# Optimization experiments

Measured on AMD Instinct MI355X. Metric: run time of the kernel, lower is better.

Reference implementation:

```python
import jax, jax.numpy as jnp
import numpy as np

H = 128  # DECODER_LAYERS[0]
LN_EPS = 1e-3  # keras LayerNormalization default epsilon


def setup_inputs() -> dict:
    key = jax.random.key(0)
    ks = jax.random.split(key, 12)
    N_POS, N_COL, D = 1024, 512, 128
    n_seq = 8
    s = 1.0 / np.sqrt(D)
    h = 1.0 / np.sqrt(H)
    return {
        "seq_feat": jax.random.normal(ks[0], (N_POS, D), jnp.float32),
        "col_feat": jax.random.normal(ks[1], (N_COL, D), jnp.float32),
        "sequence_lengths": jnp.full((n_seq,), N_POS // n_seq, dtype=jnp.int32),
        "Ws": jax.random.normal(ks[2], (D, H), jnp.float32) * s,
        "bs": jnp.zeros((H,), jnp.float32),
        "Wc": jax.random.normal(ks[3], (D, H), jnp.float32) * s,
        "bc": jnp.zeros((H,), jnp.float32),
        "Wm": jax.random.normal(ks[4], (H, H), jnp.float32) * h,
        "bm": jnp.zeros((H,), jnp.float32),
        "gamma": jnp.ones((H,), jnp.float32),
        "beta": jnp.zeros((H,), jnp.float32),
        "Wo": jax.random.normal(ks[5], (H, 1), jnp.float32) * h,
        "bo": jnp.zeros((1,), jnp.float32),
    }


def reference(seq_feat, col_feat, sequence_lengths, Ws, bs, Wc, bc, Wm, bm, gamma, beta, Wo, bo):
    N_POS = seq_feat.shape[0]
    N_COL = col_feat.shape[0]
    n_seq = sequence_lengths.shape[0]

    seq_dec = jax.nn.relu(seq_feat @ Ws + bs)   # [N_pos, H]
    col_dec = jax.nn.relu(col_feat @ Wc + bc)   # [N_col, H]

    # broadcast outer-sum: [N_pos, N_col, H]
    logits = seq_dec[:, None, :] + col_dec[None, :, :]

    # MLP([128]): single Dense (no activation) + LayerNorm
    hmid = logits @ Wm + bm
    mu = jnp.mean(hmid, axis=-1, keepdims=True)
    var = jnp.mean(jnp.square(hmid - mu), axis=-1, keepdims=True)
    hln = (hmid - mu) / jnp.sqrt(var + LN_EPS) * gamma + beta

    raw = (hln @ Wo + bo)[..., 0]               # [N_pos, N_col]
    exp_logits = jnp.exp(raw)

    # column-axis normalization (softmax over last axis)
    M_c = exp_logits / jnp.sum(exp_logits, axis=-1, keepdims=True)

    # segment-ragged normalization over positions, per sequence
    segment_ids = jnp.repeat(jnp.arange(n_seq, dtype=jnp.int32), sequence_lengths,
                             total_repeat_length=N_POS)
    seg = jax.ops.segment_sum(exp_logits, segment_ids, num_segments=n_seq)  # [n_seq, N_col]
    M_s = exp_logits / seg[segment_ids]

    return M_c + M_s - M_c * M_s
```

## Files before the change

### kernel.cpp

```cpp
#include <hip/hip_runtime.h>

#define HDIM 128
#define NPOS 1024
#define NCOL 512
#define LN_EPS 1e-3f


__device__ __forceinline__ int seg_of(int i, const int* __restrict__ lens, int n_seq) {
    int cum = 0;
    for (int s = 0; s < n_seq; ++s) {
        cum += lens[s];
        if (i < cum) return s;
    }
    return n_seq - 1;
}

extern "C" __global__ void __launch_bounds__(512)
k1_precompute(const float* __restrict__ seq_feat, const float* __restrict__ col_feat,
              const float* __restrict__ Ws, const float* __restrict__ bsv,
              const float* __restrict__ Wc, const float* __restrict__ bcv,
              const float* __restrict__ Wm, const float* __restrict__ bmv,
              const float* __restrict__ gam, const float* __restrict__ Wo,
              const int* __restrict__ lens, int n_seq,
              float* __restrict__ AcT, float* __restrict__ BcT,
              float* __restrict__ p_arr, float* __restrict__ v_arr,
              float* __restrict__ q_arr, float* __restrict__ w_arr,
              float* __restrict__ sums, int* __restrict__ segid)
{
    __shared__ float xs[4][HDIM];
    __shared__ float ds_[4][HDIM];
    __shared__ float partm[8], partp[8], partv[8], mus[4];

    const int t    = threadIdx.x;
    const int b    = blockIdx.x;
    const int h    = t & 127;
    const int r    = t >> 7;
    const int wv   = t >> 6;
    const int lane = t & 63;

    {
        const int nsums = NPOS + n_seq * NCOL;
        int idx = b * 512 + t;
        if (idx < nsums) sums[idx] = 0.f;
        int idx2 = idx - nsums;
        if (idx2 >= 0 && idx2 < NPOS) segid[idx2] = seg_of(idx2, lens, n_seq);
    }

    const bool  is_seq = (b < NPOS / 4);
    const int   i0 = (is_seq ? b : (b - NPOS / 4)) * 4;
    const float* X  = is_seq ? seq_feat : col_feat;
    const float* W1 = is_seq ? Ws : Wc;
    const float* b1 = is_seq ? bsv : bcv;

    if (t < 128) {
        int rr = t >> 5, k4 = (t & 31) * 4;
        *(float4*)&xs[rr][k4] = *(const float4*)&X[(i0 + rr) * HDIM + k4];
    }
    __syncthreads();

    float d;
    {
        float a0 = 0.f, a1 = 0.f, a2 = 0.f, a3 = 0.f;
        #pragma unroll 8
        for (int k = 0; k < HDIM; k += 4) {
            float4 x = *(const float4*)&xs[r][k];
            float w0 = W1[(k + 0) * HDIM + h];
            float w1 = W1[(k + 1) * HDIM + h];
            float w2 = W1[(k + 2) * HDIM + h];
            float w3 = W1[(k + 3) * HDIM + h];
            a0 += x.x * w0; a1 += x.y * w1; a2 += x.z * w2; a3 += x.w * w3;
        }
        d = fmaxf(b1[h] + ((a0 + a1) + (a2 + a3)), 0.f);
    }
    ds_[r][h] = d;
    __syncthreads();

    float aa;
    {
        float a0 = 0.f, a1 = 0.f, a2 = 0.f, a3 = 0.f;
        #pragma unroll 8
        for (int k = 0; k < HDIM; k += 4) {
            float4 x = *(const float4*)&ds_[r][k];
            float w0 = Wm[(k + 0) * HDIM + h];
            float w1 = Wm[(k + 1) * HDIM + h];
            float w2 = Wm[(k + 2) * HDIM + h];
            float w3 = Wm[(k + 3) * HDIM + h];
            a0 += x.x * w0; a1 += x.y * w1; a2 += x.z * w2; a3 += x.w * w3;
        }
        aa = (is_seq ? 0.f : bmv[h]) + ((a0 + a1) + (a2 + a3));
    }

    {
        float s = aa;
        #pragma unroll
        for (int off = 32; off; off >>= 1) s += __shfl_xor(s, off, 64);
        if (lane == 0) partm[wv] = s;
    }
    __syncthreads();
    if (t < 4) mus[t] = (partm[2 * t] + partm[2 * t + 1]) * (1.f / HDIM);
    __syncthreads();

    const float a  = aa - mus[r];
    const float gw = gam[h] * Wo[h];

    {
        float sp = a * gw, sv = a * a;
        #pragma unroll
        for (int off = 32; off; off >>= 1) {
            sp += __shfl_xor(sp, off, 64);
            sv += __shfl_xor(sv, off, 64);
        }
        if (lane == 0) { partp[wv] = sp; partv[wv] = sv; }
    }
    xs[r][h] = a;
    __syncthreads();
    if (t < 4) {
        (is_seq ? p_arr : q_arr)[i0 + t] = partp[2 * t] + partp[2 * t + 1];
        (is_seq ? v_arr : w_arr)[i0 + t] = (partv[2 * t] + partv[2 * t + 1]) * (1.f / HDIM);
    }
    if (t < 128) {
        float4 st = make_float4(xs[0][t], xs[1][t], xs[2][t], xs[3][t]);
        if (is_seq) *(float4*)&AcT[t * NPOS + i0] = st;
        else        *(float4*)&BcT[t * NCOL + i0] = st;
    }
}

#define AS_STR 36
#define BS_STR 68

union K2Smem {
    struct { float As[128 * AS_STR]; float Bs[128 * BS_STR]; } s;
    struct { float comb[8 * 256]; float redr[512]; float redc[1024]; } r;
};

extern "C" __global__ void __launch_bounds__(512)
k2_gemm(const float* __restrict__ AcT, const float* __restrict__ BcT,
        const float* __restrict__ p_arr, const float* __restrict__ v_arr,
        const float* __restrict__ q_arr, const float* __restrict__ w_arr,
        const int* __restrict__ segid, int n_seq,
        float* __restrict__ E, float* __restrict__ rowsum, float* __restrict__ segsum)
{
    __shared__ K2Smem sm;

    const int t  = threadIdx.x;
    const int tt = t & 255;
    const int tc = tt & 15;
    const int tr = tt >> 4;
    const int kbase = (t >> 8) * 64;
    const int i0 = blockIdx.x * 32;
    const int j0 = blockIdx.y * 64;

    #pragma unroll
    for (int u = 0; u < 2; ++u) {
        int fid = t + 512 * u;
        int k = fid >> 3, m4 = fid & 7;
        *(float4*)&sm.s.As[k * AS_STR + 4 * m4] = *(const float4*)&AcT[k * NPOS + i0 + 4 * m4];
    }
    #pragma unroll
    for (int u = 0; u < 4; ++u) {
        int fid = t + 512 * u;
        int k = fid >> 4, n4 = fid & 15;
        *(float4*)&sm.s.Bs[k * BS_STR + 4 * n4] = *(const float4*)&BcT[k * NCOL + j0 + 4 * n4];
    }
    __syncthreads();

    float acc[8] = {0.f, 0.f, 0.f, 0.f, 0.f, 0.f, 0.f, 0.f};
    #pragma unroll 4
    for (int k = kbase; k < kbase + 64; ++k) {
        float2 a2 = *(const float2*)&sm.s.As[k * AS_STR + 2 * tr];
        float4 b4 = *(const float4*)&sm.s.Bs[k * BS_STR + 4 * tc];
        acc[0] += a2.x * b4.x; acc[1] += a2.x * b4.y; acc[2] += a2.x * b4.z; acc[3] += a2.x * b4.w;
        acc[4] += a2.y * b4.x; acc[5] += a2.y * b4.y; acc[6] += a2.y * b4.z; acc[7] += a2.y * b4.w;
    }

    const int seg_lo = segid[i0];
    const int seg_hi = segid[i0 + 31];
    __syncthreads();

    if (t >= 256) {
        #pragma unroll
        for (int j = 0; j < 8; ++j) sm.r.comb[j * 256 + tt] = acc[j];
    }
    __syncthreads();

    float e[2][4];
    if (t < 256) {
        #pragma unroll
        for (int j = 0; j < 8; ++j) acc[j] += sm.r.comb[j * 256 + tt];

        const int jj = j0 + 4 * tc;
        float4 q4 = *(const float4*)&q_arr[jj];
        float4 w4 = *(const float4*)&w_arr[jj];
        float rs[2];
        #pragma unroll
        for (int mm = 0; mm < 2; ++mm) {
            const int i = i0 + 2 * tr + mm;
            const float pi = p_arr[i];
            const float vi = v_arr[i];
            e[mm][0] = __expf((pi + q4.x) * rsqrtf(vi + w4.x + acc[4*mm+0] * (2.f/HDIM) + LN_EPS));
            e[mm][1] = __expf((pi + q4.y) * rsqrtf(vi + w4.y + acc[4*mm+1] * (2.f/HDIM) + LN_EPS));
            e[mm][2] = __expf((pi + q4.z) * rsqrtf(vi + w4.z + acc[4*mm+2] * (2.f/HDIM) + LN_EPS));
            e[mm][3] = __expf((pi + q4.w) * rsqrtf(vi + w4.w + acc[4*mm+3] * (2.f/HDIM) + LN_EPS));
            rs[mm] = e[mm][0] + e[mm][1] + e[mm][2] + e[mm][3];
            *(float4*)&E[i * NCOL + jj] = make_float4(e[mm][0], e[mm][1], e[mm][2], e[mm][3]);
        }
        sm.r.redr[(2 * tr + 0) * 16 + tc] = rs[0];
        sm.r.redr[(2 * tr + 1) * 16 + tc] = rs[1];
        #pragma unroll
        for (int u = 0; u < 4; ++u)
            sm.r.redc[(4 * tc + u) * 16 + tr] = e[0][u] + e[1][u];
    }
    __syncthreads();

    if (t < 32) {
        float s = 0.f;
        #pragma unroll
        for (int m = 0; m < 16; ++m) s += sm.r.redr[t * 16 + m];
        atomicAdd(&rowsum[i0 + t], s);
    } else if (t >= 32 && t < 96 && seg_lo == seg_hi) {
        int c = t - 32;
        float s = 0.f;
        #pragma unroll
        for (int m = 0; m < 16; ++m) s += sm.r.redc[c * 16 + m];
        atomicAdd(&segsum[seg_lo * NCOL + j0 + c], s);
    }
    if (seg_lo != seg_hi && t < 256) {
        #pragma unroll
        for (int mm = 0; mm < 2; ++mm) {
            const int i = i0 + 2 * tr + mm;
            const int sg = segid[i];
            #pragma unroll
            for (int u = 0; u < 4; ++u)
                atomicAdd(&segsum[sg * NCOL + j0 + 4 * tc + u], e[mm][u]);
        }
    }
}

extern "C" __global__ void __launch_bounds__(256)
k3_final(const float* __restrict__ E, const float* __restrict__ rowsum,
         const float* __restrict__ segsum, const int* __restrict__ segid,
         float* __restrict__ out)
{
    const int gid = blockIdx.x * 256 + threadIdx.x;
    const int i = gid >> 7;
    const int j = (gid & 127) * 4;

    float4 e4 = *(const float4*)&E[i * NCOL + j];
    const float invr = 1.f / rowsum[i];
    const int sg = segid[i];
    float4 s4 = *(const float4*)&segsum[sg * NCOL + j];

    float4 o;
    { float mc = e4.x * invr, ms = e4.x / s4.x; o.x = mc + ms - mc * ms; }
    { float mc = e4.y * invr, ms = e4.y / s4.y; o.y = mc + ms - mc * ms; }
    { float mc = e4.z * invr, ms = e4.z / s4.z; o.z = mc + ms - mc * ms; }
    { float mc = e4.w * invr, ms = e4.w / s4.w; o.w = mc + ms - mc * ms; }
    *(float4*)&out[i * NCOL + j] = o;
}

extern "C" void kernel_launch(void* const* d_in, const int* in_sizes, int n_in,
                              void* d_out, int out_size, void* d_ws, size_t ws_size,
                              hipStream_t stream) {
    const float* seq_feat = (const float*)d_in[0];
    const float* col_feat = (const float*)d_in[1];
    const int*   lens     = (const int*)d_in[2];
    const float* Ws   = (const float*)d_in[3];
    const float* bs   = (const float*)d_in[4];
    const float* Wc   = (const float*)d_in[5];
    const float* bc   = (const float*)d_in[6];
    const float* Wm   = (const float*)d_in[7];
    const float* bm   = (const float*)d_in[8];
    const float* gam  = (const float*)d_in[9];
    const float* Wo   = (const float*)d_in[11];
    float* out = (float*)d_out;
    const int n_seq = in_sizes[2];

    float* ws     = (float*)d_ws;
    float* AcT    = ws;
    float* BcT    = AcT + HDIM * NPOS;
    float* p      = BcT + HDIM * NCOL;
    float* v      = p + NPOS;
    float* q      = v + NPOS;
    float* w      = q + NCOL;
    float* sums   = w + NCOL;
    float* rowsum = sums;
    float* segsum = sums + NPOS;
    float* E      = segsum + n_seq * NCOL;
    int*   segid  = (int*)(E + NPOS * NCOL);

    hipLaunchKernelGGL(k1_precompute, dim3(NPOS / 4 + NCOL / 4), dim3(512), 0, stream,
                       seq_feat, col_feat, Ws, bs, Wc, bc, Wm, bm, gam, Wo,
                       lens, n_seq, AcT, BcT, p, v, q, w, sums, segid);
    hipLaunchKernelGGL(k2_gemm, dim3(NPOS / 32, NCOL / 64), dim3(512), 0, stream,
                       AcT, BcT, p, v, q, w, segid, n_seq, E, rowsum, segsum);
    hipLaunchKernelGGL(k3_final, dim3((NPOS * NCOL / 4) / 256), dim3(256), 0, stream,
                       E, rowsum, segsum, segid, out);
}
```

Before: 100.9 us.

## Fuse three kernels into one cooperative kernel with grid syncs, keeping exps in registers

```diff
diff --git a/kernel.cpp b/kernel.cpp
--- a/kernel.cpp
+++ b/kernel.cpp
@@ -1,10 +1,25 @@
 #include <hip/hip_runtime.h>
+#include <hip/hip_cooperative_groups.h>
+
+namespace cg = cooperative_groups;
 
 #define HDIM 128
 #define NPOS 1024
 #define NCOL 512
 #define LN_EPS 1e-3f
-
+#define AS_STR 36
+#define BS_STR 68
+
+
+union Smem {
+    struct {
+        float xs[4][HDIM];
+        float ds[4][HDIM];
+        float partm[8], partp[8], partv[8], mus[4];
+    } p1;
+    struct { float As[128 * AS_STR]; float Bs[128 * BS_STR]; } s;
+    struct { float comb[8 * 256]; float redr[512]; float redc[1024]; } r;
+};
 
 __device__ __forceinline__ int seg_of(int i, const int* __restrict__ lens, int n_seq) {
     int cum = 0;
@@ -16,20 +31,20 @@
 }
 
 extern "C" __global__ void __launch_bounds__(512)
-k1_precompute(const float* __restrict__ seq_feat, const float* __restrict__ col_feat,
-              const float* __restrict__ Ws, const float* __restrict__ bsv,
-              const float* __restrict__ Wc, const float* __restrict__ bcv,
-              const float* __restrict__ Wm, const float* __restrict__ bmv,
-              const float* __restrict__ gam, const float* __restrict__ Wo,
-              const int* __restrict__ lens, int n_seq,
-              float* __restrict__ AcT, float* __restrict__ BcT,
-              float* __restrict__ p_arr, float* __restrict__ v_arr,
-              float* __restrict__ q_arr, float* __restrict__ w_arr,
-              float* __restrict__ sums, int* __restrict__ segid)
+fused(const float* __restrict__ seq_feat, const float* __restrict__ col_feat,
+      const float* __restrict__ Ws, const float* __restrict__ bsv,
+      const float* __restrict__ Wc, const float* __restrict__ bcv,
+      const float* __restrict__ Wm, const float* __restrict__ bmv,
+      const float* __restrict__ gam, const float* __restrict__ Wo,
+      const int* __restrict__ lens, int n_seq,
+      float* __restrict__ AcT, float* __restrict__ BcT,
+      float* __restrict__ p_arr, float* __restrict__ v_arr,
+      float* __restrict__ q_arr, float* __restrict__ w_arr,
+      float* __restrict__ rowsum, float* __restrict__ segsum,
+      int* __restrict__ segid, float* __restrict__ out)
 {
-    __shared__ float xs[4][HDIM];
-    __shared__ float ds_[4][HDIM];
-    __shared__ float partm[8], partp[8], partv[8], mus[4];
+    __shared__ Smem sm;
+    cg::grid_group grid = cg::this_grid();
 
     const int t    = threadIdx.x;
     const int b    = blockIdx.x;
@@ -41,114 +56,103 @@
     {
         const int nsums = NPOS + n_seq * NCOL;
         int idx = b * 512 + t;
-        if (idx < nsums) sums[idx] = 0.f;
+        if (idx < nsums) (idx < NPOS ? rowsum : segsum)[idx < NPOS ? idx : idx - NPOS] = 0.f;
         int idx2 = idx - nsums;
         if (idx2 >= 0 && idx2 < NPOS) segid[idx2] = seg_of(idx2, lens, n_seq);
     }
 
-    const bool  is_seq = (b < NPOS / 4);
-    const int   i0 = (is_seq ? b : (b - NPOS / 4)) * 4;
-    const float* X  = is_seq ? seq_feat : col_feat;
-    const float* W1 = is_seq ? Ws : Wc;
-    const float* b1 = is_seq ? bsv : bcv;
-
-    if (t < 128) {
-        int rr = t >> 5, k4 = (t & 31) * 4;
-        *(float4*)&xs[rr][k4] = *(const float4*)&X[(i0 + rr) * HDIM + k4];
-    }
-    __syncthreads();
-
-    float d;
-    {
-        float a0 = 0.f, a1 = 0.f, a2 = 0.f, a3 = 0.f;
-        #pragma unroll 8
-        for (int k = 0; k < HDIM; k += 4) {
-            float4 x = *(const float4*)&xs[r][k];
-            float w0 = W1[(k + 0) * HDIM + h];
-            float w1 = W1[(k + 1) * HDIM + h];
-            float w2 = W1[(k + 2) * HDIM + h];
-            float w3 = W1[(k + 3) * HDIM + h];
-            a0 += x.x * w0; a1 += x.y * w1; a2 += x.z * w2; a3 += x.w * w3;
-        }
-        d = fmaxf(b1[h] + ((a0 + a1) + (a2 + a3)), 0.f);
-    }
-    ds_[r][h] = d;
-    __syncthreads();
-
-    float aa;
-    {
-        float a0 = 0.f, a1 = 0.f, a2 = 0.f, a3 = 0.f;
-        #pragma unroll 8
-        for (int k = 0; k < HDIM; k += 4) {
-            float4 x = *(const float4*)&ds_[r][k];
-            float w0 = Wm[(k + 0) * HDIM + h];
-            float w1 = Wm[(k + 1) * HDIM + h];
-            float w2 = Wm[(k + 2) * HDIM + h];
-            float w3 = Wm[(k + 3) * HDIM + h];
-            a0 += x.x * w0; a1 += x.y * w1; a2 += x.z * w2; a3 += x.w * w3;
-        }
-        aa = (is_seq ? 0.f : bmv[h]) + ((a0 + a1) + (a2 + a3));
-    }
-
-    {
-        float s = aa;
-        #pragma unroll
-        for (int off = 32; off; off >>= 1) s += __shfl_xor(s, off, 64);
-        if (lane == 0) partm[wv] = s;
-    }
-    __syncthreads();
-    if (t < 4) mus[t] = (partm[2 * t] + partm[2 * t + 1]) * (1.f / HDIM);
-    __syncthreads();
-
-    const float a  = aa - mus[r];
-    const float gw = gam[h] * Wo[h];
-
-    {
-        float sp = a * gw, sv = a * a;
-        #pragma unroll
-        for (int off = 32; off; off >>= 1) {
-            sp += __shfl_xor(sp, off, 64);
-            sv += __shfl_xor(sv, off, 64);
-        }
-        if (lane == 0) { partp[wv] = sp; partv[wv] = sv; }
-    }
-    xs[r][h] = a;
-    __syncthreads();
-    if (t < 4) {
-        (is_seq ? p_arr : q_arr)[i0 + t] = partp[2 * t] + partp[2 * t + 1];
-        (is_seq ? v_arr : w_arr)[i0 + t] = (partv[2 * t] + partv[2 * t + 1]) * (1.f / HDIM);
-    }
-    if (t < 128) {
-        float4 st = make_float4(xs[0][t], xs[1][t], xs[2][t], xs[3][t]);
-        if (is_seq) *(float4*)&AcT[t * NPOS + i0] = st;
-        else        *(float4*)&BcT[t * NCOL + i0] = st;
-    }
-}
-
-#define AS_STR 36
-#define BS_STR 68
-
-union K2Smem {
-    struct { float As[128 * AS_STR]; float Bs[128 * BS_STR]; } s;
-    struct { float comb[8 * 256]; float redr[512]; float redc[1024]; } r;
-};
-
-extern "C" __global__ void __launch_bounds__(512)
-k2_gemm(const float* __restrict__ AcT, const float* __restrict__ BcT,
-        const float* __restrict__ p_arr, const float* __restrict__ v_arr,
-        const float* __restrict__ q_arr, const float* __restrict__ w_arr,
-        const int* __restrict__ segid, int n_seq,
-        float* __restrict__ E, float* __restrict__ rowsum, float* __restrict__ segsum)
-{
-    __shared__ K2Smem sm;
-
-    const int t  = threadIdx.x;
+    for (int g = b; g < (NPOS + NCOL) / 4; g += 256) {
+        const bool  is_seq = (g < NPOS / 4);
+        const int   i0 = (is_seq ? g : (g - NPOS / 4)) * 4;
+        const float* X  = is_seq ? seq_feat : col_feat;
+        const float* W1 = is_seq ? Ws : Wc;
+        const float* b1 = is_seq ? bsv : bcv;
+
+        if (t < 128) {
+            int rr = t >> 5, k4 = (t & 31) * 4;
+            *(float4*)&sm.p1.xs[rr][k4] = *(const float4*)&X[(i0 + rr) * HDIM + k4];
+        }
+        __syncthreads();
+
+        float d;
+        {
+            float a0 = 0.f, a1 = 0.f, a2 = 0.f, a3 = 0.f;
+            #pragma unroll 8
+            for (int k = 0; k < HDIM; k += 4) {
+                float4 x = *(const float4*)&sm.p1.xs[r][k];
+                float w0 = W1[(k + 0) * HDIM + h];
+                float w1 = W1[(k + 1) * HDIM + h];
+                float w2 = W1[(k + 2) * HDIM + h];
+                float w3 = W1[(k + 3) * HDIM + h];
+                a0 += x.x * w0; a1 += x.y * w1; a2 += x.z * w2; a3 += x.w * w3;
+            }
+            d = fmaxf(b1[h] + ((a0 + a1) + (a2 + a3)), 0.f);
+        }
+        sm.p1.ds[r][h] = d;
+        __syncthreads();
+
+        float aa;
+        {
+            float a0 = 0.f, a1 = 0.f, a2 = 0.f, a3 = 0.f;
+            #pragma unroll 8
+            for (int k = 0; k < HDIM; k += 4) {
+                float4 x = *(const float4*)&sm.p1.ds[r][k];
+                float w0 = Wm[(k + 0) * HDIM + h];
+                float w1 = Wm[(k + 1) * HDIM + h];
+                float w2 = Wm[(k + 2) * HDIM + h];
+                float w3 = Wm[(k + 3) * HDIM + h];
+                a0 += x.x * w0; a1 += x.y * w1; a2 += x.z * w2; a3 += x.w * w3;
+            }
+            aa = (is_seq ? 0.f : bmv[h]) + ((a0 + a1) + (a2 + a3));
+        }
+
+        {
+            float s = aa;
+            #pragma unroll
+            for (int off = 32; off; off >>= 1) s += __shfl_xor(s, off, 64);
+            if (lane == 0) sm.p1.partm[wv] = s;
+        }
+        __syncthreads();
+        if (t < 4) sm.p1.mus[t] = (sm.p1.partm[2 * t] + sm.p1.partm[2 * t + 1]) * (1.f / HDIM);
+        __syncthreads();
+
+        const float a  = aa - sm.p1.mus[r];
+        const float gw = gam[h] * Wo[h];
+
+        {
+            float sp = a * gw, sv = a * a;
+            #pragma unroll
+            for (int off = 32; off; off >>= 1) {
+                sp += __shfl_xor(sp, off, 64);
+                sv += __shfl_xor(sv, off, 64);
+            }
+            if (lane == 0) { sm.p1.partp[wv] = sp; sm.p1.partv[wv] = sv; }
+        }
+        sm.p1.xs[r][h] = a;
+        __syncthreads();
+        if (t < 4) {
+            (is_seq ? p_arr : q_arr)[i0 + t] = sm.p1.partp[2 * t] + sm.p1.partp[2 * t + 1];
+            (is_seq ? v_arr : w_arr)[i0 + t] =
+                (sm.p1.partv[2 * t] + sm.p1.partv[2 * t + 1]) * (1.f / HDIM);
+        }
+        if (t < 128) {
+            float4 st = make_float4(sm.p1.xs[0][t], sm.p1.xs[1][t], sm.p1.xs[2][t], sm.p1.xs[3][t]);
+            if (is_seq) *(float4*)&AcT[t * NPOS + i0] = st;
+            else        *(float4*)&BcT[t * NCOL + i0] = st;
+        }
+        __syncthreads();
+    }
+
+    __threadfence();
+    grid.sync();
+
     const int tt = t & 255;
     const int tc = tt & 15;
     const int tr = tt >> 4;
     const int kbase = (t >> 8) * 64;
-    const int i0 = blockIdx.x * 32;
-    const int j0 = blockIdx.y * 64;
+    const int i0 = (b & 31) * 32;
+    const int j0 = (b >> 5) * 64;
+    const int jj = j0 + 4 * tc;
 
     #pragma unroll
     for (int u = 0; u < 2; ++u) {
@@ -188,7 +192,6 @@
         #pragma unroll
         for (int j = 0; j < 8; ++j) acc[j] += sm.r.comb[j * 256 + tt];
 
-        const int jj = j0 + 4 * tc;
         float4 q4 = *(const float4*)&q_arr[jj];
         float4 w4 = *(const float4*)&w_arr[jj];
         float rs[2];
@@ -202,7 +205,6 @@
             e[mm][2] = __expf((pi + q4.z) * rsqrtf(vi + w4.z + acc[4*mm+2] * (2.f/HDIM) + LN_EPS));
             e[mm][3] = __expf((pi + q4.w) * rsqrtf(vi + w4.w + acc[4*mm+3] * (2.f/HDIM) + LN_EPS));
             rs[mm] = e[mm][0] + e[mm][1] + e[mm][2] + e[mm][3];
-            *(float4*)&E[i * NCOL + jj] = make_float4(e[mm][0], e[mm][1], e[mm][2], e[mm][3]);
         }
         sm.r.redr[(2 * tr + 0) * 16 + tc] = rs[0];
         sm.r.redr[(2 * tr + 1) * 16 + tc] = rs[1];
@@ -231,31 +233,28 @@
             const int sg = segid[i];
             #pragma unroll
             for (int u = 0; u < 4; ++u)
-                atomicAdd(&segsum[sg * NCOL + j0 + 4 * tc + u], e[mm][u]);
-        }
-    }
-}
-
-extern "C" __global__ void __launch_bounds__(256)
-k3_final(const float* __restrict__ E, const float* __restrict__ rowsum,
-         const float* __restrict__ segsum, const int* __restrict__ segid,
-         float* __restrict__ out)
-{
-    const int gid = blockIdx.x * 256 + threadIdx.x;
-    const int i = gid >> 7;
-    const int j = (gid & 127) * 4;
-
-    float4 e4 = *(const float4*)&E[i * NCOL + j];
-    const float invr = 1.f / rowsum[i];
-    const int sg = segid[i];
-    float4 s4 = *(const float4*)&segsum[sg * NCOL + j];
-
-    float4 o;
-    { float mc = e4.x * invr, ms = e4.x / s4.x; o.x = mc + ms - mc * ms; }
-    { float mc = e4.y * invr, ms = e4.y / s4.y; o.y = mc + ms - mc * ms; }
-    { float mc = e4.z * invr, ms = e4.z / s4.z; o.z = mc + ms - mc * ms; }
-    { float mc = e4.w * invr, ms = e4.w / s4.w; o.w = mc + ms - mc * ms; }
-    *(float4*)&out[i * NCOL + j] = o;
+                atomicAdd(&segsum[sg * NCOL + jj + u], e[mm][u]);
+        }
+    }
+
+    __threadfence();
+    grid.sync();
+
+    if (t < 256) {
+        #pragma unroll
+        for (int mm = 0; mm < 2; ++mm) {
+            const int i = i0 + 2 * tr + mm;
+            const float invr = 1.f / rowsum[i];
+            const int sg = segid[i];
+            float4 s4 = *(const float4*)&segsum[sg * NCOL + jj];
+            float4 o;
+            { float mc = e[mm][0] * invr, ms = e[mm][0] / s4.x; o.x = mc + ms - mc * ms; }
+            { float mc = e[mm][1] * invr, ms = e[mm][1] / s4.y; o.y = mc + ms - mc * ms; }
+            { float mc = e[mm][2] * invr, ms = e[mm][2] / s4.z; o.z = mc + ms - mc * ms; }
+            { float mc = e[mm][3] * invr, ms = e[mm][3] / s4.w; o.w = mc + ms - mc * ms; }
+            *(float4*)&out[i * NCOL + jj] = o;
+        }
+    }
 }
 
 extern "C" void kernel_launch(void* const* d_in, const int* in_sizes, int n_in,
@@ -273,7 +272,7 @@
     const float* gam  = (const float*)d_in[9];
     const float* Wo   = (const float*)d_in[11];
     float* out = (float*)d_out;
-    const int n_seq = in_sizes[2];
+    int n_seq = in_sizes[2];
 
     float* ws     = (float*)d_ws;
     float* AcT    = ws;
@@ -282,17 +281,15 @@
     float* v      = p + NPOS;
     float* q      = v + NPOS;
     float* w      = q + NCOL;
-    float* sums   = w + NCOL;
-    float* rowsum = sums;
-    float* segsum = sums + NPOS;
-    float* E      = segsum + n_seq * NCOL;
-    int*   segid  = (int*)(E + NPOS * NCOL);
-
-    hipLaunchKernelGGL(k1_precompute, dim3(NPOS / 4 + NCOL / 4), dim3(512), 0, stream,
-                       seq_feat, col_feat, Ws, bs, Wc, bc, Wm, bm, gam, Wo,
-                       lens, n_seq, AcT, BcT, p, v, q, w, sums, segid);
-    hipLaunchKernelGGL(k2_gemm, dim3(NPOS / 32, NCOL / 64), dim3(512), 0, stream,
-                       AcT, BcT, p, v, q, w, segid, n_seq, E, rowsum, segsum);
-    hipLaunchKernelGGL(k3_final, dim3((NPOS * NCOL / 4) / 256), dim3(256), 0, stream,
-                       E, rowsum, segsum, segid, out);
+    float* rowsum = w + NCOL;
+    float* segsum = rowsum + NPOS;
+    int*   segid  = (int*)(segsum + n_seq * NCOL);
+
+    void* args[] = {
+        (void*)&seq_feat, (void*)&col_feat, (void*)&Ws, (void*)&bs, (void*)&Wc, (void*)&bc,
+        (void*)&Wm, (void*)&bm, (void*)&gam, (void*)&Wo, (void*)&lens, (void*)&n_seq,
+        (void*)&AcT, (void*)&BcT, (void*)&p, (void*)&v, (void*)&q, (void*)&w,
+        (void*)&rowsum, (void*)&segsum, (void*)&segid, (void*)&out
+    };
+    hipLaunchCooperativeKernel((void*)fused, dim3(256), dim3(512), args, 0, stream);
 }
```

Result: slower. 252.1 us (+149.8%).
